# Kernel tuning notes

Hardware: AMD Instinct MI355X
Metric: run time of the kernel (lower is better)

Reference implementation:

```python
import jax, jax.numpy as jnp
import numpy as np

N = 100000   # nodes
E = 600000   # edges
D = 128      # d_model / hidden_dim
L = 4        # num_layers
V = 5000     # node vocab (in_size)
G = 128      # num graphs in batch
C = 10       # num_class
BN_EPS = 1e-5


def setup_inputs() -> dict:
    key = jax.random.key(0)
    ks = jax.random.split(key, 20)
    s = 0.05
    return {
        "x": jax.random.randint(ks[0], (N,), 0, V),
        "edge_index": jax.random.randint(ks[1], (2, E), 0, N),
        "edge_attr": jax.random.normal(ks[2], (E, 2), dtype=jnp.float32),
        "batch": jnp.sort(jax.random.randint(ks[3], (N,), 0, G)),
        # embedding table
        "emb": jax.random.normal(ks[4], (V, D), dtype=jnp.float32) * s,
        # per-layer GINEConv edge linear (edge_dim=2 -> D)
        "edge_w": jax.random.normal(ks[5], (L, 2, D), dtype=jnp.float32) * s,
        "edge_b": jnp.zeros((L, D), jnp.float32),
        # per-layer MLP: Linear -> BN -> ReLU -> Linear
        "w1": jax.random.normal(ks[6], (L, D, D), dtype=jnp.float32) * s,
        "b1": jnp.zeros((L, D), jnp.float32),
        "g1": jnp.ones((L, D), jnp.float32),
        "beta1": jnp.zeros((L, D), jnp.float32),
        "w2": jax.random.normal(ks[7], (L, D, D), dtype=jnp.float32) * s,
        "b2": jnp.zeros((L, D), jnp.float32),
        # per-layer outer BatchNorm (self.norms)
        "ng": jnp.ones((L, D), jnp.float32),
        "nb": jnp.zeros((L, D), jnp.float32),
        # classifier: Linear(D,D) -> ReLU -> Linear(D,C)
        "cw1": jax.random.normal(ks[8], (D, D), dtype=jnp.float32) * s,
        "cb1": jnp.zeros((D,), jnp.float32),
        "cw2": jax.random.normal(ks[9], (D, C), dtype=jnp.float32) * s,
        "cb2": jnp.zeros((C,), jnp.float32),
    }


def _bn(h, g, b):
    # training-mode BatchNorm1d over node axis, biased variance
    m = h.mean(0)
    v = h.var(0)
    return (h - m) * jax.lax.rsqrt(v + BN_EPS) * g + b


def reference(x, edge_index, edge_attr, batch, emb, edge_w, edge_b,
              w1, b1, g1, beta1, w2, b2, ng, nb, cw1, cb1, cw2, cb2):
    h = emb[x]                                    # [N, D]
    src, dst = edge_index[0], edge_index[1]
    for l in range(L):
        e = edge_attr @ edge_w[l] + edge_b[l]     # [E, D]
        msg = jax.nn.relu(h[src] + e)             # gather + add + relu
        agg = jax.ops.segment_sum(msg, dst, num_segments=N)  # scatter-sum
        z = h + agg                               # (1+eps)*x_i + aggr, eps=0
        z = jax.nn.relu(_bn(z @ w1[l] + b1[l], g1[l], beta1[l]))
        h = _bn(z @ w2[l] + b2[l], ng[l], nb[l])
        if l != L - 1:
            h = jax.nn.relu(h)
    sums = jax.ops.segment_sum(h, batch, num_segments=G)            # [G, D]
    counts = jax.ops.segment_sum(jnp.ones((N, 1), h.dtype), batch, num_segments=G)
    pooled = sums / jnp.maximum(counts, 1.0)      # global mean pool
    return jax.nn.relu(pooled @ cw1 + cb1) @ cw2 + cb2  # [G, C]
```

## Files before the change

### kernel.cpp

```cpp
#include <hip/hip_runtime.h>
#include <stdint.h>

#define N_NODES 100000
#define N_EDGES 600000
#define DMODEL  128
#define NLAYERS 4
#define NGRAPH  128
#define NCLASS  10
#define BN_EPS  1e-5f
#define NSLOT   32

typedef __bf16 bf16x8 __attribute__((ext_vector_type(8)));
typedef __bf16 bf16x2 __attribute__((ext_vector_type(2)));
typedef float  f32x4  __attribute__((ext_vector_type(4)));

__global__ void k_zero(int* __restrict__ deg, float* __restrict__ statpart,
                       float* __restrict__ psum) {
  int i = blockIdx.x * 256 + threadIdx.x;
  if (i < N_NODES) deg[i] = 0;
  if (i < NSLOT * 2 * DMODEL) statpart[i] = 0.0f;
  if (i < NGRAPH * DMODEL) psum[i] = 0.0f;
}

__global__ void k_embed(const int* __restrict__ x, const float* __restrict__ emb,
                        __bf16* __restrict__ h) {
  int idx = blockIdx.x * 256 + threadIdx.x;
  if (idx >= N_NODES * DMODEL / 2) return;
  int i = idx >> 6;
  int p = idx & 63;
  float2 v = *(const float2*)(emb + (size_t)x[i] * DMODEL + p * 2);
  bf16x2 o;
  o[0] = (__bf16)v.x;
  o[1] = (__bf16)v.y;
  *(bf16x2*)(h + (size_t)i * DMODEL + p * 2) = o;
}

__global__ void k_cvtw(const float* __restrict__ w1, const float* __restrict__ w2,
                       __bf16* __restrict__ wt_hi, __bf16* __restrict__ wt_lo) {
  int idx = blockIdx.x * 256 + threadIdx.x;
  if (idx >= NLAYERS * 2 * DMODEL * DMODEL) return;
  int mat = idx >> 14;
  int rem = idx & 16383;
  int n = rem >> 7;
  int k = rem & 127;
  int l = mat >> 1;
  int which = mat & 1;
  const float* w = which ? w2 : w1;
  float v = w[(size_t)l * DMODEL * DMODEL + (size_t)k * DMODEL + n];
  __bf16 hi = (__bf16)v;
  wt_hi[idx] = hi;
  wt_lo[idx] = (__bf16)(v - (float)hi);
}

__global__ void k_hist(const int* __restrict__ dst, int* __restrict__ deg) {
  int e = blockIdx.x * 256 + threadIdx.x;
  if (e < N_EDGES) atomicAdd(&deg[dst[e]], 1);
}

__global__ void k_scan1(const int* __restrict__ deg, int* __restrict__ out,
                        int* __restrict__ bsum, int n) {
  __shared__ int lds[256];
  int t = threadIdx.x;
  int idx = blockIdx.x * 256 + t;
  int v = (idx < n) ? deg[idx] : 0;
  int val = v;
  lds[t] = val;
  for (int ofs = 1; ofs < 256; ofs <<= 1) {
    __syncthreads();
    int u = (t >= ofs) ? lds[t - ofs] : 0;
    __syncthreads();
    val += u;
    lds[t] = val;
  }
  if (idx < n) out[idx] = val - v;
  if (t == 255) bsum[blockIdx.x] = val;
}

__global__ void k_scan2(const int* __restrict__ bsum, int* __restrict__ bsumx, int nb) {
  __shared__ int lds[512];
  int t = threadIdx.x;
  int v = (t < nb) ? bsum[t] : 0;
  int val = v;
  lds[t] = val;
  for (int ofs = 1; ofs < 512; ofs <<= 1) {
    __syncthreads();
    int u = (t >= ofs) ? lds[t - ofs] : 0;
    __syncthreads();
    val += u;
    lds[t] = val;
  }
  if (t < nb) bsumx[t] = val - v;
}

__global__ void k_scan3(int* __restrict__ row_start, int* __restrict__ cursor,
                        const int* __restrict__ bsumx, int n, int total) {
  int idx = blockIdx.x * 256 + threadIdx.x;
  if (idx < n) {
    int v = row_start[idx] + bsumx[blockIdx.x];
    row_start[idx] = v;
    cursor[idx] = v;
  }
  if (idx == 0) row_start[n] = total;
}

__global__ void k_scatter(const int* __restrict__ ei, const float* __restrict__ ea,
                          int* __restrict__ cursor, int4* __restrict__ epack) {
  int e = blockIdx.x * 256 + threadIdx.x;
  if (e >= N_EDGES) return;
  int s = ei[e];
  int d = ei[N_EDGES + e];
  int pos = atomicAdd(&cursor[d], 1);
  int4 pk;
  pk.x = s;
  pk.y = __float_as_int(ea[2 * e]);
  pk.z = __float_as_int(ea[2 * e + 1]);
  pk.w = 0;
  epack[pos] = pk;
}

__global__ void __launch_bounds__(256) k_agg(
    const __bf16* __restrict__ h, const int* __restrict__ row_start,
    const int4* __restrict__ epack,
    const float* __restrict__ ew,
    const float* __restrict__ ebp,
    const float* __restrict__ sIn, const float* __restrict__ tIn, int hasT,
    __bf16* __restrict__ z) {
  int node = blockIdx.x * 4 + (threadIdx.x >> 6);
  if (node >= N_NODES) return;
  int lane = threadIdx.x & 63;
  int d0 = lane * 2;

  float ew0a = ew[d0],          ew0b = ew[d0 + 1];
  float ew1a = ew[DMODEL + d0], ew1b = ew[DMODEL + d0 + 1];
  float eba = ebp[d0],          ebb = ebp[d0 + 1];
  float sa = 1.0f, ta = 0.0f, sb = 1.0f, tb = 0.0f;
  if (hasT) {
    sa = sIn[d0]; ta = tIn[d0];
    sb = sIn[d0 + 1]; tb = tIn[d0 + 1];
  }

  bf16x2 hv = *(const bf16x2*)(h + (size_t)node * DMODEL + d0);
  float r0 = (float)hv[0];
  float r1 = (float)hv[1];
  float acc0 = hasT ? fmaxf(sa * r0 + ta, 0.0f) : r0;
  float acc1 = hasT ? fmaxf(sb * r1 + tb, 0.0f) : r1;

  int j0 = row_start[node];
  int j1 = row_start[node + 1];
  int j = j0;

#define AGG_ONE(E, V)                                                          \
  {                                                                            \
    float a0 = __int_as_float((E).y);                                          \
    float a1 = __int_as_float((E).z);                                          \
    float f0 = (float)(V)[0];                                                  \
    float f1 = (float)(V)[1];                                                  \
    if (hasT) {                                                                \
      f0 = fmaxf(sa * f0 + ta, 0.0f);                                          \
      f1 = fmaxf(sb * f1 + tb, 0.0f);                                          \
    }                                                                          \
    acc0 += fmaxf(f0 + a0 * ew0a + a1 * ew1a + eba, 0.0f);                     \
    acc1 += fmaxf(f1 + a0 * ew0b + a1 * ew1b + ebb, 0.0f);                     \
  }

  for (; j + 4 <= j1; j += 4) {
    int4 e0 = epack[j];
    int4 e1 = epack[j + 1];
    int4 e2 = epack[j + 2];
    int4 e3 = epack[j + 3];
    bf16x2 v0 = *(const bf16x2*)(h + (size_t)e0.x * DMODEL + d0);
    bf16x2 v1 = *(const bf16x2*)(h + (size_t)e1.x * DMODEL + d0);
    bf16x2 v2 = *(const bf16x2*)(h + (size_t)e2.x * DMODEL + d0);
    bf16x2 v3 = *(const bf16x2*)(h + (size_t)e3.x * DMODEL + d0);
    AGG_ONE(e0, v0)
    AGG_ONE(e1, v1)
    AGG_ONE(e2, v2)
    AGG_ONE(e3, v3)
  }
  for (; j < j1; ++j) {
    int4 e0 = epack[j];
    bf16x2 v0 = *(const bf16x2*)(h + (size_t)e0.x * DMODEL + d0);
    AGG_ONE(e0, v0)
  }
#undef AGG_ONE

  bf16x2 o;
  o[0] = (__bf16)acc0;
  o[1] = (__bf16)acc1;
  *(bf16x2*)(z + (size_t)node * DMODEL + d0) = o;
}

__global__ void __launch_bounds__(256) k_gemm(
    const __bf16* __restrict__ X,
    const __bf16* __restrict__ Whi, const __bf16* __restrict__ Wlo,
    const float* __restrict__ bias,
    const float* __restrict__ sIn, const float* __restrict__ tIn, int applyIn,
    __bf16* __restrict__ Y,
    float* __restrict__ statpart) {
  int tid = threadIdx.x;
  int wave = tid >> 6;
  int lane = tid & 63;
  int n16 = lane & 15;
  int quad = lane >> 4;

  bf16x8 bhi[2][4];
  bf16x8 blo[2][4];
#pragma unroll
  for (int ct = 0; ct < 2; ++ct) {
    int n = (wave * 2 + ct) * 16 + n16;
#pragma unroll
    for (int kk = 0; kk < 4; ++kk) {
      int k0 = kk * 32 + quad * 8;
      bhi[ct][kk] = *(const bf16x8*)(Whi + (size_t)n * DMODEL + k0);
      blo[ct][kk] = *(const bf16x8*)(Wlo + (size_t)n * DMODEL + k0);
    }
  }
  float bc[2];
  bc[0] = bias[(wave * 2 + 0) * 16 + n16];
  bc[1] = bias[(wave * 2 + 1) * 16 + n16];

  float ssum[2] = {0.0f, 0.0f};
  float ssq[2] = {0.0f, 0.0f};

  const int NCHUNK = N_NODES / 32;
  for (int c = blockIdx.x; c < NCHUNK; c += gridDim.x) {
    int row0 = c * 32;
    bf16x8 a[2][4];
#pragma unroll
    for (int t = 0; t < 2; ++t) {
      const __bf16* xr = X + (size_t)(row0 + t * 16 + n16) * DMODEL;
#pragma unroll
      for (int kk = 0; kk < 4; ++kk) {
        a[t][kk] = *(const bf16x8*)(xr + kk * 32 + quad * 8);
      }
    }
    if (applyIn) {
#pragma unroll
      for (int kk = 0; kk < 4; ++kk) {
        int k0 = kk * 32 + quad * 8;
        float4 s0 = *(const float4*)(sIn + k0);
        float4 s1 = *(const float4*)(sIn + k0 + 4);
        float4 t0 = *(const float4*)(tIn + k0);
        float4 t1 = *(const float4*)(tIn + k0 + 4);
        float sv[8];
        float tv[8];
        sv[0] = s0.x; sv[1] = s0.y; sv[2] = s0.z; sv[3] = s0.w;
        sv[4] = s1.x; sv[5] = s1.y; sv[6] = s1.z; sv[7] = s1.w;
        tv[0] = t0.x; tv[1] = t0.y; tv[2] = t0.z; tv[3] = t0.w;
        tv[4] = t1.x; tv[5] = t1.y; tv[6] = t1.z; tv[7] = t1.w;
#pragma unroll
        for (int t = 0; t < 2; ++t) {
#pragma unroll
          for (int jj = 0; jj < 8; ++jj) {
            float f = (float)a[t][kk][jj];
            a[t][kk][jj] = (__bf16)fmaxf(sv[jj] * f + tv[jj], 0.0f);
          }
        }
      }
    }

    f32x4 acc[2][2];
#pragma unroll
    for (int t = 0; t < 2; ++t)
#pragma unroll
      for (int ct = 0; ct < 2; ++ct)
#pragma unroll
        for (int r = 0; r < 4; ++r) acc[t][ct][r] = 0.0f;

#pragma unroll
    for (int kk = 0; kk < 4; ++kk) {
#pragma unroll
      for (int ct = 0; ct < 2; ++ct) {
#pragma unroll
        for (int t = 0; t < 2; ++t) {
          acc[t][ct] = __builtin_amdgcn_mfma_f32_16x16x32_bf16(a[t][kk], bhi[ct][kk], acc[t][ct], 0, 0, 0);
          acc[t][ct] = __builtin_amdgcn_mfma_f32_16x16x32_bf16(a[t][kk], blo[ct][kk], acc[t][ct], 0, 0, 0);
        }
      }
    }

#pragma unroll
    for (int t = 0; t < 2; ++t) {
#pragma unroll
      for (int ct = 0; ct < 2; ++ct) {
        int col = (wave * 2 + ct) * 16 + n16;
#pragma unroll
        for (int r = 0; r < 4; ++r) {
          int row = row0 + t * 16 + quad * 4 + r;
          float v = acc[t][ct][r] + bc[ct];
          Y[(size_t)row * DMODEL + col] = (__bf16)v;
          ssum[ct] += v;
          ssq[ct] += v * v;
        }
      }
    }
  }

  int slot = blockIdx.x & (NSLOT - 1);
#pragma unroll
  for (int ct = 0; ct < 2; ++ct) {
    int col = (wave * 2 + ct) * 16 + n16;
    float s = ssum[ct];
    float q = ssq[ct];
    s += __shfl_xor(s, 16);
    q += __shfl_xor(q, 16);
    s += __shfl_xor(s, 32);
    q += __shfl_xor(q, 32);
    if (quad == 0) {
      atomicAdd(&statpart[slot * (2 * DMODEL) + col], s);
      atomicAdd(&statpart[slot * (2 * DMODEL) + DMODEL + col], q);
    }
  }
}

__global__ void k_bnfin(float* __restrict__ statpart,
                        const float* __restrict__ gamma, const float* __restrict__ beta,
                        float* __restrict__ sOut, float* __restrict__ tOut) {
  int d = threadIdx.x;
  float sum = 0.0f;
  float sq = 0.0f;
  for (int p = 0; p < NSLOT; ++p) {
    sum += statpart[p * (2 * DMODEL) + d];
    sq  += statpart[p * (2 * DMODEL) + DMODEL + d];
  }
  float mean = sum * (1.0f / N_NODES);
  float var = sq * (1.0f / N_NODES) - mean * mean;
  float inv = rsqrtf(var + BN_EPS);
  float s = gamma[d] * inv;
  sOut[d] = s;
  tOut[d] = beta[d] - mean * s;
  for (int p = 0; p < NSLOT; ++p) {
    statpart[p * (2 * DMODEL) + d] = 0.0f;
    statpart[p * (2 * DMODEL) + DMODEL + d] = 0.0f;
  }
}

__global__ void k_gstart(const int* __restrict__ batch, int* __restrict__ gstart) {
  int g = blockIdx.x * 256 + threadIdx.x;
  if (g > NGRAPH) return;
  int lo = 0;
  int hi = N_NODES;
  while (lo < hi) {
    int mid = (lo + hi) >> 1;
    if (batch[mid] < g) lo = mid + 1; else hi = mid;
  }
  gstart[g] = lo;
}

__global__ void k_pool(const __bf16* __restrict__ h, const int* __restrict__ gstart,
                       float* __restrict__ psum) {
  int g = blockIdx.x;
  int slice = blockIdx.y;
  int lane = threadIdx.x;
  int d0 = lane * 2;
  int i0 = gstart[g];
  int i1 = gstart[g + 1];
  float a0 = 0.0f;
  float a1 = 0.0f;
  for (int i = i0 + slice; i < i1; i += 8) {
    bf16x2 v = *(const bf16x2*)(h + (size_t)i * DMODEL + d0);
    a0 += (float)v[0];
    a1 += (float)v[1];
  }
  atomicAdd(&psum[g * DMODEL + d0], a0);
  atomicAdd(&psum[g * DMODEL + d0 + 1], a1);
}

__global__ void k_classifier(const float* __restrict__ psum, const int* __restrict__ gstart,
                             const float* __restrict__ s2, const float* __restrict__ t2,
                             const float* __restrict__ cw1, const float* __restrict__ cb1,
                             const float* __restrict__ cw2, const float* __restrict__ cb2,
                             float* __restrict__ out) {
  __shared__ float pl[DMODEL];
  __shared__ float hid[DMODEL];
  int g = blockIdx.x;
  int d = threadIdx.x;
  int cnt = gstart[g + 1] - gstart[g];
  pl[d] = (cnt > 0) ? (s2[d] * (psum[g * DMODEL + d] / (float)cnt) + t2[d]) : 0.0f;
  __syncthreads();
  float acc = cb1[d];
  for (int k = 0; k < DMODEL; ++k) acc += pl[k] * cw1[k * DMODEL + d];
  hid[d] = fmaxf(acc, 0.0f);
  __syncthreads();
  if (d < NCLASS) {
    float acc2 = cb2[d];
    for (int k = 0; k < DMODEL; ++k) acc2 += hid[k] * cw2[k * NCLASS + d];
    out[g * NCLASS + d] = acc2;
  }
}

extern "C" void kernel_launch(void* const* d_in, const int* in_sizes, int n_in,
                              void* d_out, int out_size, void* d_ws, size_t ws_size,
                              hipStream_t stream) {
  const int*   x      = (const int*)d_in[0];
  const int*   ei     = (const int*)d_in[1];
  const float* ea     = (const float*)d_in[2];
  const int*   batch  = (const int*)d_in[3];
  const float* emb    = (const float*)d_in[4];
  const float* edge_w = (const float*)d_in[5];
  const float* edge_b = (const float*)d_in[6];
  const float* w1     = (const float*)d_in[7];
  const float* b1     = (const float*)d_in[8];
  const float* g1     = (const float*)d_in[9];
  const float* beta1  = (const float*)d_in[10];
  const float* w2     = (const float*)d_in[11];
  const float* b2     = (const float*)d_in[12];
  const float* ng     = (const float*)d_in[13];
  const float* nb     = (const float*)d_in[14];
  const float* cw1    = (const float*)d_in[15];
  const float* cb1    = (const float*)d_in[16];
  const float* cw2    = (const float*)d_in[17];
  const float* cb2    = (const float*)d_in[18];

  char* ws = (char*)d_ws;
  size_t off = 0;
  auto alloc = [&](size_t bytes) -> void* {
    void* p = ws + off;
    off += (bytes + 255) & ~(size_t)255;
    return p;
  };

  __bf16* h_bf      = (__bf16*)alloc((size_t)N_NODES * DMODEL * sizeof(__bf16));
  __bf16* z_bf      = (__bf16*)alloc((size_t)N_NODES * DMODEL * sizeof(__bf16));
  __bf16* y1_bf     = (__bf16*)alloc((size_t)N_NODES * DMODEL * sizeof(__bf16));
  int*    row_start = (int*)alloc((N_NODES + 1) * sizeof(int));
  int*    cursor    = (int*)alloc(N_NODES * sizeof(int));
  int*    deg       = (int*)alloc(N_NODES * sizeof(int));
  int4*   epack     = (int4*)alloc((size_t)N_EDGES * sizeof(int4));
  __bf16* wt_hi     = (__bf16*)alloc((size_t)NLAYERS * 2 * DMODEL * DMODEL * sizeof(__bf16));
  __bf16* wt_lo     = (__bf16*)alloc((size_t)NLAYERS * 2 * DMODEL * DMODEL * sizeof(__bf16));
  float*  statpart  = (float*)alloc((size_t)NSLOT * 2 * DMODEL * sizeof(float));
  float*  st        = (float*)alloc((size_t)NLAYERS * 2 * 2 * DMODEL * sizeof(float));
  int*    gstart    = (int*)alloc((NGRAPH + 1) * sizeof(int));
  float*  psum      = (float*)alloc((size_t)NGRAPH * DMODEL * sizeof(float));
  int*    bsum      = (int*)alloc(512 * sizeof(int));
  int*    bsumx     = (int*)alloc(512 * sizeof(int));

  auto sArr = [&](int l, int which) { return st + ((l * 2 + which) * 2 + 0) * DMODEL; };
  auto tArr = [&](int l, int which) { return st + ((l * 2 + which) * 2 + 1) * DMODEL; };

  const int nbScan = (N_NODES + 255) / 256;
  const int nbEdge = (N_EDGES + 255) / 256;
  const int nbEmb  = (N_NODES * DMODEL / 2 + 255) / 256;
  const int nbGemm = 782;
  const int nbAgg  = (N_NODES + 3) / 4;

  k_zero<<<nbScan, 256, 0, stream>>>(deg, statpart, psum);
  k_embed<<<nbEmb, 256, 0, stream>>>(x, emb, h_bf);
  k_cvtw<<<(NLAYERS * 2 * DMODEL * DMODEL) / 256, 256, 0, stream>>>(w1, w2, wt_hi, wt_lo);
  k_hist<<<nbEdge, 256, 0, stream>>>(ei + N_EDGES, deg);
  k_scan1<<<nbScan, 256, 0, stream>>>(deg, row_start, bsum, N_NODES);
  k_scan2<<<1, 512, 0, stream>>>(bsum, bsumx, nbScan);
  k_scan3<<<nbScan, 256, 0, stream>>>(row_start, cursor, bsumx, N_NODES, N_EDGES);
  k_scatter<<<nbEdge, 256, 0, stream>>>(ei, ea, cursor, epack);
  k_gstart<<<1, 256, 0, stream>>>(batch, gstart);

  for (int l = 0; l < NLAYERS; ++l) {
    const float* sI = (l > 0) ? sArr(l - 1, 1) : (const float*)nullptr;
    const float* tI = (l > 0) ? tArr(l - 1, 1) : (const float*)nullptr;
    k_agg<<<nbAgg, 256, 0, stream>>>(h_bf, row_start, epack,
                                     edge_w + (size_t)l * 2 * DMODEL,
                                     edge_b + (size_t)l * DMODEL,
                                     sI, tI, (l > 0) ? 1 : 0, z_bf);
    k_gemm<<<nbGemm, 256, 0, stream>>>(
        z_bf,
        wt_hi + (size_t)(l * 2 + 0) * DMODEL * DMODEL,
        wt_lo + (size_t)(l * 2 + 0) * DMODEL * DMODEL,
        b1 + (size_t)l * DMODEL,
        (const float*)nullptr, (const float*)nullptr, 0,
        y1_bf, statpart);
    k_bnfin<<<1, DMODEL, 0, stream>>>(statpart,
                                      g1 + (size_t)l * DMODEL, beta1 + (size_t)l * DMODEL,
                                      sArr(l, 0), tArr(l, 0));
    k_gemm<<<nbGemm, 256, 0, stream>>>(
        y1_bf,
        wt_hi + (size_t)(l * 2 + 1) * DMODEL * DMODEL,
        wt_lo + (size_t)(l * 2 + 1) * DMODEL * DMODEL,
        b2 + (size_t)l * DMODEL,
        sArr(l, 0), tArr(l, 0), 1,
        h_bf, statpart);
    k_bnfin<<<1, DMODEL, 0, stream>>>(statpart,
                                      ng + (size_t)l * DMODEL, nb + (size_t)l * DMODEL,
                                      sArr(l, 1), tArr(l, 1));
  }

  dim3 poolGrid(NGRAPH, 8);
  k_pool<<<poolGrid, 64, 0, stream>>>(h_bf, gstart, psum);
  k_classifier<<<NGRAPH, DMODEL, 0, stream>>>(psum, gstart, sArr(NLAYERS - 1, 1),
                                              tArr(NLAYERS - 1, 1),
                                              cw1, cb1, cw2, cb2, (float*)d_out);
}
```

Baseline: 713.5 us.

## Stage GEMM output through LDS for coalesced stores and prefetch next A tile

The GEMM epilogue now writes fp32 results into a double-buffered LDS tile, then each thread emits 16-byte bf16x8 rows, replacing scattered 2-byte global stores. The next chunk's A operand is loaded from global memory right after the barrier, before the store phase, so the load latency overlaps the writeback. This adds about 34 KB of LDS per block and a __syncthreads per chunk, which may lower occupancy.

```diff
diff --git a/kernel.cpp b/kernel.cpp
--- a/kernel.cpp
+++ b/kernel.cpp
@@ -197,6 +197,7 @@
     const float* __restrict__ sIn, const float* __restrict__ tIn, int applyIn,
     __bf16* __restrict__ Y,
     float* __restrict__ statpart) {
+  __shared__ __align__(16) float cstage[2][32 * 132];
   int tid = threadIdx.x;
   int wave = tid >> 6;
   int lane = tid & 63;
@@ -223,17 +224,23 @@
   float ssq[2] = {0.0f, 0.0f};
 
   const int NCHUNK = N_NODES / 32;
-  for (int c = blockIdx.x; c < NCHUNK; c += gridDim.x) {
-    int row0 = c * 32;
-    bf16x8 a[2][4];
-#pragma unroll
-    for (int t = 0; t < 2; ++t) {
-      const __bf16* xr = X + (size_t)(row0 + t * 16 + n16) * DMODEL;
-#pragma unroll
-      for (int kk = 0; kk < 4; ++kk) {
-        a[t][kk] = *(const bf16x8*)(xr + kk * 32 + quad * 8);
-      }
-    }
+  int buf = 0;
+  int c = blockIdx.x;
+
+  bf16x8 a[2][4];
+  {
+    const __bf16* xb = X + (size_t)c * 32 * DMODEL;
+#pragma unroll
+    for (int t = 0; t < 2; ++t)
+#pragma unroll
+      for (int kk = 0; kk < 4; ++kk)
+        a[t][kk] = *(const bf16x8*)(xb + (t * 16 + n16) * DMODEL + kk * 32 + quad * 8);
+  }
+
+  while (c < NCHUNK) {
+    int cn = c + gridDim.x;
+    if (cn >= NCHUNK) cn = c;
+
     if (applyIn) {
 #pragma unroll
       for (int kk = 0; kk < 4; ++kk) {
@@ -279,6 +286,7 @@
       }
     }
 
+    float* cs = &cstage[buf][0];
 #pragma unroll
     for (int t = 0; t < 2; ++t) {
 #pragma unroll
@@ -286,14 +294,39 @@
         int col = (wave * 2 + ct) * 16 + n16;
 #pragma unroll
         for (int r = 0; r < 4; ++r) {
-          int row = row0 + t * 16 + quad * 4 + r;
           float v = acc[t][ct][r] + bc[ct];
-          Y[(size_t)row * DMODEL + col] = (__bf16)v;
+          cs[(t * 16 + quad * 4 + r) * 132 + col] = v;
           ssum[ct] += v;
           ssq[ct] += v * v;
         }
       }
     }
+    __syncthreads();
+
+    {
+      const __bf16* xb = X + (size_t)cn * 32 * DMODEL;
+#pragma unroll
+      for (int t = 0; t < 2; ++t)
+#pragma unroll
+        for (int kk = 0; kk < 4; ++kk)
+          a[t][kk] = *(const bf16x8*)(xb + (t * 16 + n16) * DMODEL + kk * 32 + quad * 8);
+    }
+
+    int row0 = c * 32;
+#pragma unroll
+    for (int p = 0; p < 2; ++p) {
+      int r = p * 16 + (tid >> 4);
+      int c0 = (tid & 15) * 8;
+      float4 v0 = *(const float4*)(cs + r * 132 + c0);
+      float4 v1 = *(const float4*)(cs + r * 132 + c0 + 4);
+      bf16x8 o;
+      o[0] = (__bf16)v0.x; o[1] = (__bf16)v0.y; o[2] = (__bf16)v0.z; o[3] = (__bf16)v0.w;
+      o[4] = (__bf16)v1.x; o[5] = (__bf16)v1.y; o[6] = (__bf16)v1.z; o[7] = (__bf16)v1.w;
+      *(bf16x8*)(Y + (size_t)(row0 + r) * DMODEL + c0) = o;
+    }
+
+    buf ^= 1;
+    c += gridDim.x;
   }
 
   int slot = blockIdx.x & (NSLOT - 1);
```

Measured after the change: 736.0 us. 1.03x slower.

## Fuse BN finalize into GEMM via last-block ticket, prefetch rows, merge init kernels

Applied to the files above, without the earlier changes.

Removes the separate BN-finalize kernel launches by having the last GEMM block (detected by an atomic ticket) reduce the per-slot statistics and write the scale/shift. Merges zero-init, weight conversion and graph-start search into one init kernel. Restructures the GEMM to 16-row chunks with a doubled grid and software-prefetches the next chunk's A tile. This trades fewer launches and better latency hiding for per-block ticket atomics and fences, and for half the MFMA work per iteration.

```diff
diff --git a/kernel.cpp b/kernel.cpp
--- a/kernel.cpp
+++ b/kernel.cpp
@@ -14,12 +14,38 @@
 typedef __bf16 bf16x2 __attribute__((ext_vector_type(2)));
 typedef float  f32x4  __attribute__((ext_vector_type(4)));
 
-__global__ void k_zero(int* __restrict__ deg, float* __restrict__ statpart,
-                       float* __restrict__ psum) {
+__global__ void k_init(int* __restrict__ deg, float* __restrict__ statpart,
+                       float* __restrict__ psum, int* __restrict__ ticket,
+                       const float* __restrict__ w1, const float* __restrict__ w2,
+                       __bf16* __restrict__ wt_hi, __bf16* __restrict__ wt_lo,
+                       const int* __restrict__ batch, int* __restrict__ gstart) {
   int i = blockIdx.x * 256 + threadIdx.x;
   if (i < N_NODES) deg[i] = 0;
   if (i < NSLOT * 2 * DMODEL) statpart[i] = 0.0f;
   if (i < NGRAPH * DMODEL) psum[i] = 0.0f;
+  if (i == 0) *ticket = 0;
+  {
+    int mat = i >> 14;
+    int rem = i & 16383;
+    int n = rem >> 7;
+    int k = rem & 127;
+    int l = mat >> 1;
+    int which = mat & 1;
+    const float* w = which ? w2 : w1;
+    float v = w[(size_t)l * DMODEL * DMODEL + (size_t)k * DMODEL + n];
+    __bf16 hi = (__bf16)v;
+    wt_hi[i] = hi;
+    wt_lo[i] = (__bf16)(v - (float)hi);
+  }
+  if (i <= NGRAPH) {
+    int lo = 0;
+    int hi = N_NODES;
+    while (lo < hi) {
+      int mid = (lo + hi) >> 1;
+      if (batch[mid] < i) lo = mid + 1; else hi = mid;
+    }
+    gstart[i] = lo;
+  }
 }
 
 __global__ void k_embed(const int* __restrict__ x, const float* __restrict__ emb,
@@ -33,23 +59,6 @@
   o[0] = (__bf16)v.x;
   o[1] = (__bf16)v.y;
   *(bf16x2*)(h + (size_t)i * DMODEL + p * 2) = o;
-}
-
-__global__ void k_cvtw(const float* __restrict__ w1, const float* __restrict__ w2,
-                       __bf16* __restrict__ wt_hi, __bf16* __restrict__ wt_lo) {
-  int idx = blockIdx.x * 256 + threadIdx.x;
-  if (idx >= NLAYERS * 2 * DMODEL * DMODEL) return;
-  int mat = idx >> 14;
-  int rem = idx & 16383;
-  int n = rem >> 7;
-  int k = rem & 127;
-  int l = mat >> 1;
-  int which = mat & 1;
-  const float* w = which ? w2 : w1;
-  float v = w[(size_t)l * DMODEL * DMODEL + (size_t)k * DMODEL + n];
-  __bf16 hi = (__bf16)v;
-  wt_hi[idx] = hi;
-  wt_lo[idx] = (__bf16)(v - (float)hi);
 }
 
 __global__ void k_hist(const int* __restrict__ dst, int* __restrict__ deg) {
@@ -196,7 +205,10 @@
     const float* __restrict__ bias,
     const float* __restrict__ sIn, const float* __restrict__ tIn, int applyIn,
     __bf16* __restrict__ Y,
-    float* __restrict__ statpart) {
+    float* statpart,
+    const float* __restrict__ gamma, const float* __restrict__ beta,
+    float* __restrict__ sOut, float* __restrict__ tOut,
+    int* __restrict__ ticket) {
   int tid = threadIdx.x;
   int wave = tid >> 6;
   int lane = tid & 63;
@@ -222,18 +234,27 @@
   float ssum[2] = {0.0f, 0.0f};
   float ssq[2] = {0.0f, 0.0f};
 
-  const int NCHUNK = N_NODES / 32;
-  for (int c = blockIdx.x; c < NCHUNK; c += gridDim.x) {
-    int row0 = c * 32;
-    bf16x8 a[2][4];
-#pragma unroll
-    for (int t = 0; t < 2; ++t) {
-      const __bf16* xr = X + (size_t)(row0 + t * 16 + n16) * DMODEL;
-#pragma unroll
-      for (int kk = 0; kk < 4; ++kk) {
-        a[t][kk] = *(const bf16x8*)(xr + kk * 32 + quad * 8);
-      }
-    }
+  const int NCHUNK = N_NODES / 16;
+  int c = blockIdx.x;
+
+  bf16x8 a[4];
+  {
+    const __bf16* xr = X + (size_t)(c * 16 + n16) * DMODEL + quad * 8;
+#pragma unroll
+    for (int kk = 0; kk < 4; ++kk) a[kk] = *(const bf16x8*)(xr + kk * 32);
+  }
+
+  while (c < NCHUNK) {
+    int cn = c + gridDim.x;
+    int cp = (cn < NCHUNK) ? cn : c;
+
+    bf16x8 anx[4];
+    {
+      const __bf16* xr = X + (size_t)(cp * 16 + n16) * DMODEL + quad * 8;
+#pragma unroll
+      for (int kk = 0; kk < 4; ++kk) anx[kk] = *(const bf16x8*)(xr + kk * 32);
+    }
+
     if (applyIn) {
 #pragma unroll
       for (int kk = 0; kk < 4; ++kk) {
@@ -249,51 +270,45 @@
         tv[0] = t0.x; tv[1] = t0.y; tv[2] = t0.z; tv[3] = t0.w;
         tv[4] = t1.x; tv[5] = t1.y; tv[6] = t1.z; tv[7] = t1.w;
 #pragma unroll
-        for (int t = 0; t < 2; ++t) {
-#pragma unroll
-          for (int jj = 0; jj < 8; ++jj) {
-            float f = (float)a[t][kk][jj];
-            a[t][kk][jj] = (__bf16)fmaxf(sv[jj] * f + tv[jj], 0.0f);
-          }
+        for (int jj = 0; jj < 8; ++jj) {
+          float f = (float)a[kk][jj];
+          a[kk][jj] = (__bf16)fmaxf(sv[jj] * f + tv[jj], 0.0f);
         }
       }
     }
 
-    f32x4 acc[2][2];
-#pragma unroll
-    for (int t = 0; t < 2; ++t)
-#pragma unroll
-      for (int ct = 0; ct < 2; ++ct)
-#pragma unroll
-        for (int r = 0; r < 4; ++r) acc[t][ct][r] = 0.0f;
+    f32x4 acc[2];
+#pragma unroll
+    for (int ct = 0; ct < 2; ++ct)
+#pragma unroll
+      for (int r = 0; r < 4; ++r) acc[ct][r] = 0.0f;
 
 #pragma unroll
     for (int kk = 0; kk < 4; ++kk) {
 #pragma unroll
       for (int ct = 0; ct < 2; ++ct) {
-#pragma unroll
-        for (int t = 0; t < 2; ++t) {
-          acc[t][ct] = __builtin_amdgcn_mfma_f32_16x16x32_bf16(a[t][kk], bhi[ct][kk], acc[t][ct], 0, 0, 0);
-          acc[t][ct] = __builtin_amdgcn_mfma_f32_16x16x32_bf16(a[t][kk], blo[ct][kk], acc[t][ct], 0, 0, 0);
-        }
+        acc[ct] = __builtin_amdgcn_mfma_f32_16x16x32_bf16(a[kk], bhi[ct][kk], acc[ct], 0, 0, 0);
+        acc[ct] = __builtin_amdgcn_mfma_f32_16x16x32_bf16(a[kk], blo[ct][kk], acc[ct], 0, 0, 0);
       }
     }
 
-#pragma unroll
-    for (int t = 0; t < 2; ++t) {
-#pragma unroll
-      for (int ct = 0; ct < 2; ++ct) {
-        int col = (wave * 2 + ct) * 16 + n16;
-#pragma unroll
-        for (int r = 0; r < 4; ++r) {
-          int row = row0 + t * 16 + quad * 4 + r;
-          float v = acc[t][ct][r] + bc[ct];
-          Y[(size_t)row * DMODEL + col] = (__bf16)v;
-          ssum[ct] += v;
-          ssq[ct] += v * v;
-        }
+    int row0 = c * 16;
+#pragma unroll
+    for (int ct = 0; ct < 2; ++ct) {
+      int col = (wave * 2 + ct) * 16 + n16;
+#pragma unroll
+      for (int r = 0; r < 4; ++r) {
+        int row = row0 + quad * 4 + r;
+        float v = acc[ct][r] + bc[ct];
+        Y[(size_t)row * DMODEL + col] = (__bf16)v;
+        ssum[ct] += v;
+        ssq[ct] += v * v;
       }
     }
+
+#pragma unroll
+    for (int kk = 0; kk < 4; ++kk) a[kk] = anx[kk];
+    c = cn;
   }
 
   int slot = blockIdx.x & (NSLOT - 1);
@@ -311,40 +326,38 @@
       atomicAdd(&statpart[slot * (2 * DMODEL) + DMODEL + col], q);
     }
   }
-}
-
-__global__ void k_bnfin(float* __restrict__ statpart,
-                        const float* __restrict__ gamma, const float* __restrict__ beta,
-                        float* __restrict__ sOut, float* __restrict__ tOut) {
-  int d = threadIdx.x;
-  float sum = 0.0f;
-  float sq = 0.0f;
-  for (int p = 0; p < NSLOT; ++p) {
-    sum += statpart[p * (2 * DMODEL) + d];
-    sq  += statpart[p * (2 * DMODEL) + DMODEL + d];
-  }
-  float mean = sum * (1.0f / N_NODES);
-  float var = sq * (1.0f / N_NODES) - mean * mean;
-  float inv = rsqrtf(var + BN_EPS);
-  float s = gamma[d] * inv;
-  sOut[d] = s;
-  tOut[d] = beta[d] - mean * s;
-  for (int p = 0; p < NSLOT; ++p) {
-    statpart[p * (2 * DMODEL) + d] = 0.0f;
-    statpart[p * (2 * DMODEL) + DMODEL + d] = 0.0f;
-  }
-}
-
-__global__ void k_gstart(const int* __restrict__ batch, int* __restrict__ gstart) {
-  int g = blockIdx.x * 256 + threadIdx.x;
-  if (g > NGRAPH) return;
-  int lo = 0;
-  int hi = N_NODES;
-  while (lo < hi) {
-    int mid = (lo + hi) >> 1;
-    if (batch[mid] < g) lo = mid + 1; else hi = mid;
-  }
-  gstart[g] = lo;
+
+  __threadfence();
+  __shared__ int isLast;
+  __syncthreads();
+  if (tid == 0) {
+    int old = atomicAdd(ticket, 1);
+    isLast = (old == (int)gridDim.x - 1);
+  }
+  __syncthreads();
+  if (isLast) {
+    __threadfence();
+    if (tid < DMODEL) {
+      volatile float* sp = statpart;
+      float sum = 0.0f;
+      float sq = 0.0f;
+      for (int p = 0; p < NSLOT; ++p) {
+        sum += sp[p * (2 * DMODEL) + tid];
+        sq  += sp[p * (2 * DMODEL) + DMODEL + tid];
+      }
+      float mean = sum * (1.0f / N_NODES);
+      float var = sq * (1.0f / N_NODES) - mean * mean;
+      float inv = rsqrtf(var + BN_EPS);
+      float s = gamma[tid] * inv;
+      sOut[tid] = s;
+      tOut[tid] = beta[tid] - mean * s;
+      for (int p = 0; p < NSLOT; ++p) {
+        statpart[p * (2 * DMODEL) + tid] = 0.0f;
+        statpart[p * (2 * DMODEL) + DMODEL + tid] = 0.0f;
+      }
+    }
+    if (tid == 0) *ticket = 0;
+  }
 }
 
 __global__ void k_pool(const __bf16* __restrict__ h, const int* __restrict__ gstart,
@@ -433,6 +446,7 @@
   float*  st        = (float*)alloc((size_t)NLAYERS * 2 * 2 * DMODEL * sizeof(float));
   int*    gstart    = (int*)alloc((NGRAPH + 1) * sizeof(int));
   float*  psum      = (float*)alloc((size_t)NGRAPH * DMODEL * sizeof(float));
+  int*    ticket    = (int*)alloc(256);
   int*    bsum      = (int*)alloc(512 * sizeof(int));
   int*    bsumx     = (int*)alloc(512 * sizeof(int));
 
@@ -442,18 +456,17 @@
   const int nbScan = (N_NODES + 255) / 256;
   const int nbEdge = (N_EDGES + 255) / 256;
   const int nbEmb  = (N_NODES * DMODEL / 2 + 255) / 256;
-  const int nbGemm = 782;
+  const int nbGemm = 1563;
   const int nbAgg  = (N_NODES + 3) / 4;
 
-  k_zero<<<nbScan, 256, 0, stream>>>(deg, statpart, psum);
+  k_init<<<512, 256, 0, stream>>>(deg, statpart, psum, ticket,
+                                  w1, w2, wt_hi, wt_lo, batch, gstart);
   k_embed<<<nbEmb, 256, 0, stream>>>(x, emb, h_bf);
-  k_cvtw<<<(NLAYERS * 2 * DMODEL * DMODEL) / 256, 256, 0, stream>>>(w1, w2, wt_hi, wt_lo);
   k_hist<<<nbEdge, 256, 0, stream>>>(ei + N_EDGES, deg);
   k_scan1<<<nbScan, 256, 0, stream>>>(deg, row_start, bsum, N_NODES);
   k_scan2<<<1, 512, 0, stream>>>(bsum, bsumx, nbScan);
   k_scan3<<<nbScan, 256, 0, stream>>>(row_start, cursor, bsumx, N_NODES, N_EDGES);
   k_scatter<<<nbEdge, 256, 0, stream>>>(ei, ea, cursor, epack);
-  k_gstart<<<1, 256, 0, stream>>>(batch, gstart);
 
   for (int l = 0; l < NLAYERS; ++l) {
     const float* sI = (l > 0) ? sArr(l - 1, 1) : (const float*)nullptr;
@@ -468,20 +481,18 @@
         wt_lo + (size_t)(l * 2 + 0) * DMODEL * DMODEL,
         b1 + (size_t)l * DMODEL,
         (const float*)nullptr, (const float*)nullptr, 0,
-        y1_bf, statpart);
-    k_bnfin<<<1, DMODEL, 0, stream>>>(statpart,
-                                      g1 + (size_t)l * DMODEL, beta1 + (size_t)l * DMODEL,
-                                      sArr(l, 0), tArr(l, 0));
+        y1_bf, statpart,
+        g1 + (size_t)l * DMODEL, beta1 + (size_t)l * DMODEL,
+        sArr(l, 0), tArr(l, 0), ticket);
     k_gemm<<<nbGemm, 256, 0, stream>>>(
         y1_bf,
         wt_hi + (size_t)(l * 2 + 1) * DMODEL * DMODEL,
         wt_lo + (size_t)(l * 2 + 1) * DMODEL * DMODEL,
         b2 + (size_t)l * DMODEL,
         sArr(l, 0), tArr(l, 0), 1,
-        h_bf, statpart);
-    k_bnfin<<<1, DMODEL, 0, stream>>>(statpart,
-                                      ng + (size_t)l * DMODEL, nb + (size_t)l * DMODEL,
-                                      sArr(l, 1), tArr(l, 1));
+        h_bf, statpart,
+        ng + (size_t)l * DMODEL, nb + (size_t)l * DMODEL,
+        sArr(l, 1), tArr(l, 1), ticket);
   }
 
   dim3 poolGrid(NGRAPH, 8);
```

Result: slower. 2.298 ms (+222.1%).
